# Optimization experiments

Hardware: AMD Instinct MI355X
Metric: run time of the kernel (lower is better)

Reference implementation:

```python
import jax, jax.numpy as jnp
import numpy as np
import math

B, S, H, DM = 1, 2048, 16, 1024
DK = DM // H
MAX_SEQ = 2048  # rel_embed has MAX_SEQ+1 rows


def setup_inputs() -> dict:
    rng = jax.random.key(0)
    ks = jax.random.split(rng, 12)
    w = lambda k, shape, s=0.02: (jax.random.normal(k, shape, jnp.float32) * s)
    inp = {
        'query': jax.random.normal(ks[0], (B, S, DM), jnp.float32),
        'key':   jax.random.normal(ks[1], (B, S, DM), jnp.float32),
        'value': jax.random.normal(ks[2], (B, S, DM), jnp.float32),
        # causal integer mask [B,S,S] (cumsum over it derives rel-pos indices)
        'mask': jnp.broadcast_to(jnp.tril(jnp.ones((S, S), jnp.int32)), (B, S, S)),
        'Wq': w(ks[3], (DM, DM)), 'bq': jnp.zeros((DM,), jnp.float32),
        'Wk': w(ks[4], (DM, DM)), 'bk': jnp.zeros((DM,), jnp.float32),
        'Wv': w(ks[5], (DM, DM)), 'bv': jnp.zeros((DM,), jnp.float32),
        'Wo': w(ks[6], (DM, DM)), 'bo': jnp.zeros((DM,), jnp.float32),
        # relative position embeddings [h, max_seq_len+1, d_k], N(0,1) as in the module
        'rel_embed': jax.random.normal(ks[7], (H, MAX_SEQ + 1, DK), jnp.float32),
    }
    return inp


def reference(query, key, value, mask, Wq, bq, Wk, bk, Wv, bv, Wo, bo, rel_embed):
    scale = 1.0 / math.sqrt(DK)
    heads = lambda x, W, b: (x @ W.T + b).reshape(B, S, H, DK).transpose(0, 2, 1, 3)
    q = heads(query, Wq, bq)   # [B,H,S,DK]
    k = heads(key, Wk, bk)
    v = heads(value, Wv, bv)

    scores = jnp.einsum('bhid,bhjd->bhij', q, k) * scale  # [B,H,S,S]

    m4 = mask[:, None, :, :]                 # [B,1,S,S]
    nz = m4 != 0
    # torch: cumsum(mask)-1 picks the m-index; index 0 (then zeroed) where mask==0
    m_idx = jnp.where(nz, jnp.cumsum(m4, axis=-1) - 1, 0)  # [B,1,S,S]

    # rel_scores[b,h,m,l] = <q[b,h,l,:], rel_embed[h,m,:]> / sqrt(d_k)
    rel = jnp.einsum('bhld,hmd->bhml', q, rel_embed[:, :S]) * scale  # [B,H,S,S]
    idx = jnp.broadcast_to(m_idx, (B, H, S, S))
    # torch.take flat-index decodes to rel[b,h, m_idx[i,j], j]
    rel_g = jnp.take_along_axis(rel, idx, axis=2) * nz.astype(scores.dtype)

    scores = jnp.where(nz, scores + rel_g, jnp.float32(-1e9))
    p = jax.nn.softmax(scores, axis=-1)      # dropout p=0.0 -> identity

    out = jnp.einsum('bhij,bhjd->bhid', p, v)         # [B,H,S,DK]
    out = out.transpose(0, 2, 1, 3).reshape(B, S, DM)  # [B,S,DM]
    return out @ Wo.T + bo
```

## Files before the change

### kernel.cpp

```cpp
#include <hip/hip_runtime.h>

typedef __bf16 bf16_t;
typedef __bf16 bf16x4 __attribute__((ext_vector_type(4)));
typedef __bf16 bf16x8 __attribute__((ext_vector_type(8)));
typedef float  f32x4  __attribute__((ext_vector_type(4)));
typedef float  f32x16 __attribute__((ext_vector_type(16)));
typedef unsigned int u32;

#define S_LEN 2048
#define DMODEL 1024
#define NHEAD 16
#define DHEAD 64
#define RELROWS 2049

__device__ __forceinline__ void gload16(const void* g, void* l) {
    __builtin_amdgcn_global_load_lds((const __attribute__((address_space(1))) void*)g,
                                     (__attribute__((address_space(3))) void*)l,
                                     16, 0, 0);
}

__device__ __forceinline__ f32x4 mfma16(bf16x8 a, bf16x8 b, f32x4 c) {
    return __builtin_amdgcn_mfma_f32_16x16x32_bf16(a, b, c, 0, 0, 0);
}
__device__ __forceinline__ f32x16 mfma32(bf16x8 a, bf16x8 b, f32x16 c) {
    return __builtin_amdgcn_mfma_f32_32x32x16_bf16(a, b, c, 0, 0, 0);
}

__device__ __forceinline__ bf16x8 lds_read_swz(const bf16_t* base, int row, int colb) {
    return *(const bf16x8*)((const char*)base + row * 128 + (colb ^ ((row & 7) << 4)));
}

__device__ __forceinline__ u32 cvtpk(float lo, float hi) {
    u32 w;
    asm("v_cvt_pk_bf16_f32 %0, %1, %2" : "=v"(w) : "v"(lo), "v"(hi));
    return w;
}
__device__ __forceinline__ void swap32(u32& a, u32& b) {
    asm("v_permlane32_swap_b32 %0, %1" : "+v"(a), "+v"(b));
}
__device__ __forceinline__ float fexp2(float x) {
    float r;
    asm("v_exp_f32 %0, %1" : "=v"(r) : "v"(x));
    return r;
}

__global__ __launch_bounds__(256)
void f2bf_all(const float* __restrict__ xq, const float* __restrict__ xk,
              const float* __restrict__ xv,
              const float* __restrict__ wq, const float* __restrict__ wk,
              const float* __restrict__ wv, const float* __restrict__ wo,
              bf16_t* __restrict__ dst, int n4X, int n4W) {
    const int i = blockIdx.x * blockDim.x + threadIdx.x;
    const float* src; int j;
    if (i < 3 * n4X) {
        if (i < n4X)            { src = xq; j = i; }
        else if (i < 2 * n4X)   { src = xk; j = i - n4X; }
        else                    { src = xv; j = i - 2 * n4X; }
    } else {
        int w = i - 3 * n4X;
        if (w < n4W)            { src = wq; j = w; }
        else if (w < 2 * n4W)   { src = wk; j = w - n4W; }
        else if (w < 3 * n4W)   { src = wv; j = w - 2 * n4W; }
        else                    { src = wo; j = w - 3 * n4W; }
    }
    float4 v = ((const float4*)src)[j];
    bf16x4 o;
    o[0] = (bf16_t)v.x; o[1] = (bf16_t)v.y; o[2] = (bf16_t)v.z; o[3] = (bf16_t)v.w;
    ((bf16x4*)dst)[i] = o;
}

template <int BM, int BN>
__global__ __launch_bounds__(256)
void gemm_qkv(const bf16_t* __restrict__ Abase, const bf16_t* __restrict__ Wbase,
              const float* __restrict__ b0, const float* __restrict__ b1,
              const float* __restrict__ b2,
              bf16_t* __restrict__ outb,
              const float* __restrict__ relp, float* __restrict__ RGout,
              bf16_t* __restrict__ vtp,
              int M, int N, int K) {
    __shared__ alignas(16) bf16_t As[2][BM * 64];
    __shared__ alignas(16) bf16_t Bs[2][BN * 64];
    const int tid = threadIdx.x, lane = tid & 63, wave = tid >> 6;
    const int z = blockIdx.z;
    const bf16_t* A = Abase + (size_t)z * M * K;
    const bf16_t* W = Wbase + (size_t)z * N * K;
    const float* bias = (z == 0) ? b0 : (z == 1 ? b1 : b2);
    const int nwg = gridDim.x * gridDim.y;
    const int wg = blockIdx.y * gridDim.x + blockIdx.x;
    const int swz = (wg & 7) * (nwg >> 3) + (wg >> 3);
    const int m0 = (swz / gridDim.x) * BM, n0 = (swz % gridDim.x) * BN;
    const int wr = (wave >> 1) * (BM / 2), wc = (wave & 1) * (BN / 2);
    constexpr int MR = BM / 32, NR = BN / 32;
    constexpr int LOADS = BM / 32 + BN / 32;

    f32x4 acc[MR][NR] = {};
    const int soff = wave * 1024 + lane * 16;

    auto stage = [&](int b, int kt) {
#pragma unroll
        for (int r = 0; r < BM / 32; ++r) {
            int L = r * 4096 + soff;
            int row = L >> 7, colb = (L & 127) ^ ((row & 7) << 4);
            gload16(A + (size_t)(m0 + row) * K + kt + (colb >> 1),
                    (char*)As[b] + r * 4096 + wave * 1024);
        }
#pragma unroll
        for (int r = 0; r < BN / 32; ++r) {
            int L = r * 4096 + soff;
            int row = L >> 7, colb = (L & 127) ^ ((row & 7) << 4);
            gload16(W + (size_t)(n0 + row) * K + kt + (colb >> 1),
                    (char*)Bs[b] + r * 4096 + wave * 1024);
        }
    };

    const int NK = K >> 6;
    stage(0, 0);
    for (int s = 0; s < NK; ++s) {
        const int buf = s & 1;
        if (s + 1 < NK) {
            stage(buf ^ 1, (s + 1) << 6);
            if constexpr (LOADS == 6) asm volatile("s_waitcnt vmcnt(6)" ::: "memory");
            else if constexpr (LOADS == 4) asm volatile("s_waitcnt vmcnt(4)" ::: "memory");
            else asm volatile("s_waitcnt vmcnt(8)" ::: "memory");
        } else {
            asm volatile("s_waitcnt vmcnt(0)" ::: "memory");
        }
        asm volatile("s_barrier" ::: "memory");
#pragma unroll
        for (int kk = 0; kk < 2; ++kk) {
            bf16x8 af[MR], bfr[NR];
#pragma unroll
            for (int m = 0; m < MR; ++m)
                af[m] = lds_read_swz(As[buf], wr + m * 16 + (lane & 15),
                                     kk * 64 + (lane >> 4) * 16);
#pragma unroll
            for (int n = 0; n < NR; ++n)
                bfr[n] = lds_read_swz(Bs[buf], wc + n * 16 + (lane & 15),
                                      kk * 64 + (lane >> 4) * 16);
#pragma unroll
            for (int m = 0; m < MR; ++m)
#pragma unroll
                for (int n = 0; n < NR; ++n)
                    acc[m][n] = mfma16(af[m], bfr[n], acc[m][n]);
        }
        asm volatile("s_barrier" ::: "memory");
    }

    const float scale = (z == 0) ? 0.18033688011112042f : 1.0f;
    float rp[MR][4];
#pragma unroll
    for (int m = 0; m < MR; ++m)
#pragma unroll
        for (int r2 = 0; r2 < 4; ++r2) rp[m][r2] = 0.f;
    const int hh = n0 >> 6;
#pragma unroll
    for (int m = 0; m < MR; ++m) {
        const int gi = m0 + wr + m * 16 + (lane >> 4) * 4;
#pragma unroll
        for (int n = 0; n < NR; ++n) {
            const int gj = n0 + wc + n * 16 + (lane & 15);
            const float bv = bias[gj];
            if (z == 2) {
                bf16x4 o4;
#pragma unroll
                for (int r2 = 0; r2 < 4; ++r2) o4[r2] = (bf16_t)(acc[m][n][r2] + bv);
                *(bf16x4*)&vtp[(size_t)gj * S_LEN + gi] = o4;
            } else {
#pragma unroll
                for (int r2 = 0; r2 < 4; ++r2) {
                    float v = (acc[m][n][r2] + bv) * scale;
                    outb[(size_t)z * M * N + (size_t)(gi + r2) * N + gj] = (bf16_t)v;
                    if (z == 0)
                        rp[m][r2] += v * relp[((size_t)hh * RELROWS + (gi + r2)) * DHEAD + (gj & 63)];
                }
            }
        }
    }
    if (z == 0) {
        constexpr int HM = BM / 2;
        float* Rp = (float*)As;
#pragma unroll
        for (int m = 0; m < MR; ++m)
#pragma unroll
            for (int r2 = 0; r2 < 4; ++r2) {
                float p = rp[m][r2];
                p += __shfl_xor(p, 1);
                p += __shfl_xor(p, 2);
                p += __shfl_xor(p, 4);
                p += __shfl_xor(p, 8);
                if ((lane & 15) == 0)
                    Rp[wave * HM + m * 16 + (lane >> 4) * 4 + r2] = p;
            }
        __syncthreads();
        if ((wave & 1) == 0) {
#pragma unroll
            for (int rr0 = 0; rr0 < HM; rr0 += 64) {
                int rr = rr0 + lane;
                if (rr < HM) {
                    float v = Rp[wave * HM + rr] + Rp[(wave + 1) * HM + rr];
                    RGout[hh * S_LEN + m0 + wr + rr] = v;
                }
            }
        }
    }
}

__global__ __launch_bounds__(512)
void gemm_out(const bf16_t* __restrict__ A, const bf16_t* __restrict__ W,
              const float* __restrict__ bias, float* __restrict__ outf,
              int M, int N, int K) {
    __shared__ alignas(16) bf16_t As[2][2][64 * 64];
    __shared__ alignas(16) bf16_t Bs[2][2][64 * 64];
    const int tid = threadIdx.x, lane = tid & 63, wave = tid >> 6;
    const int grp = wave >> 2, w4 = wave & 3;
    const int nwg = gridDim.x * gridDim.y;
    const int wg = blockIdx.y * gridDim.x + blockIdx.x;
    const int swz = (wg & 7) * (nwg >> 3) + (wg >> 3);
    const int m0 = (swz / gridDim.x) * 64, n0 = (swz % gridDim.x) * 64;
    const int wr = (w4 >> 1) * 32, wc = (w4 & 1) * 32;
    const int kbase = grp * (K >> 1);

    f32x4 acc[2][2] = {};
    const int soff = w4 * 1024 + lane * 16;

    auto stage = [&](int b, int kt) {
#pragma unroll
        for (int r = 0; r < 2; ++r) {
            int L = r * 4096 + soff;
            int row = L >> 7, colb = (L & 127) ^ ((row & 7) << 4);
            gload16(A + (size_t)(m0 + row) * K + kt + (colb >> 1),
                    (char*)As[grp][b] + r * 4096 + w4 * 1024);
            gload16(W + (size_t)(n0 + row) * K + kt + (colb >> 1),
                    (char*)Bs[grp][b] + r * 4096 + w4 * 1024);
        }
    };

    const int NKg = K >> 7;
    stage(0, kbase);
    for (int s = 0; s < NKg; ++s) {
        const int buf = s & 1;
        if (s + 1 < NKg) {
            stage(buf ^ 1, kbase + ((s + 1) << 6));
            asm volatile("s_waitcnt vmcnt(4)" ::: "memory");
        } else {
            asm volatile("s_waitcnt vmcnt(0)" ::: "memory");
        }
        asm volatile("s_barrier" ::: "memory");
#pragma unroll
        for (int kk = 0; kk < 2; ++kk) {
            bf16x8 af[2], bfr[2];
#pragma unroll
            for (int m = 0; m < 2; ++m)
                af[m] = lds_read_swz(As[grp][buf], wr + m * 16 + (lane & 15),
                                     kk * 64 + (lane >> 4) * 16);
#pragma unroll
            for (int n = 0; n < 2; ++n)
                bfr[n] = lds_read_swz(Bs[grp][buf], wc + n * 16 + (lane & 15),
                                      kk * 64 + (lane >> 4) * 16);
#pragma unroll
            for (int m = 0; m < 2; ++m)
#pragma unroll
                for (int n = 0; n < 2; ++n)
                    acc[m][n] = mfma16(af[m], bfr[n], acc[m][n]);
        }
        asm volatile("s_barrier" ::: "memory");
    }

    float* scr = (float*)As;
    if (grp == 1) {
        float* base = scr + ((w4 * 64 + lane) << 4);
#pragma unroll
        for (int m = 0; m < 2; ++m)
#pragma unroll
            for (int n = 0; n < 2; ++n)
                *(f32x4*)(base + (m * 2 + n) * 4) = acc[m][n];
    }
    __syncthreads();
    if (grp == 0) {
        const float* base = scr + ((w4 * 64 + lane) << 4);
#pragma unroll
        for (int m = 0; m < 2; ++m) {
            const int gi = m0 + wr + m * 16 + (lane >> 4) * 4;
#pragma unroll
            for (int n = 0; n < 2; ++n) {
                f32x4 ov = *(const f32x4*)(base + (m * 2 + n) * 4);
                const int gj = n0 + wc + n * 16 + (lane & 15);
                const float bv = bias[gj];
#pragma unroll
                for (int r2 = 0; r2 < 4; ++r2)
                    outf[(size_t)(gi + r2) * N + gj] = acc[m][n][r2] + ov[r2] + bv;
            }
        }
    }
}

__global__ __launch_bounds__(256, 2)
void flash_attn(const bf16_t* __restrict__ Qb, const bf16_t* __restrict__ Kb,
                const bf16_t* __restrict__ Vtp, const float* __restrict__ RG,
                bf16_t* __restrict__ Ob) {
    __shared__ alignas(16) bf16_t KB[4][64 * 64];
    __shared__ alignas(16) bf16_t VB[4][64 * 64];
    __shared__ alignas(16) float Rs[S_LEN];
    const int tid = threadIdx.x, lane = tid & 63, wave = tid >> 6;
    const int h = blockIdx.x;
    const int qt = (int)gridDim.y - 1 - (int)blockIdx.y;
    const int q0 = qt * 32;
    const int nt = (qt >> 1) + 1;
    const int qpar = qt & 1;
    const int lo5 = lane & 31, hi = lane >> 5;

    const int nkv = nt * 64;
    for (int i = tid * 8; i < nkv; i += 2048) {
        *(float4*)&Rs[i]     = *(const float4*)&RG[h * S_LEN + i];
        *(float4*)&Rs[i + 4] = *(const float4*)&RG[h * S_LEN + i + 4];
    }

    const bf16_t* qp = Qb + (size_t)(q0 + lo5) * DMODEL + h * DHEAD;
    bf16x8 qf[4];
#pragma unroll
    for (int c = 0; c < 4; ++c)
        qf[c] = *(const bf16x8*)(qp + c * 16 + hi * 8);

    auto stageK = [&](int tt) {
        char* dst = (char*)KB[wave];
#pragma unroll
        for (int rr = 0; rr < 8; ++rr) {
            int L = rr * 1024 + lane * 16;
            int row = L >> 7, colb = (L & 127) ^ ((row & 7) << 4);
            gload16(Kb + (size_t)(tt * 64 + row) * DMODEL + h * DHEAD + (colb >> 1),
                    dst + rr * 1024);
        }
    };
    auto stageV = [&](int tt) {
        char* dst = (char*)VB[wave];
#pragma unroll
        for (int rr = 0; rr < 8; ++rr) {
            int L = rr * 1024 + lane * 16;
            int row = L >> 7, colb = (L & 127) ^ ((row & 7) << 4);
            gload16(Vtp + (size_t)(h * DHEAD + row) * S_LEN + tt * 64 + (colb >> 1),
                    dst + rr * 1024);
        }
    };

    if (wave < nt) { stageK(wave); stageV(wave); }
    __syncthreads();

    f32x16 oacc[2] = {};
    float ls = 0.f;
    const int thr = qpar * 32 + lo5;

    for (int tt = wave; tt < nt; tt += 4) {
        const int kv0 = tt * 64;
        const bool diag = (tt == nt - 1);
        asm volatile("s_waitcnt vmcnt(8)" ::: "memory");

        f32x16 sta, stb;
#pragma unroll
        for (int g = 0; g < 4; ++g) {
            f32x4 ra = *(const f32x4*)&Rs[kv0 + g * 8 + hi * 4];
            f32x4 rb = *(const f32x4*)&Rs[kv0 + 32 + g * 8 + hi * 4];
#pragma unroll
            for (int e = 0; e < 4; ++e) { sta[g * 4 + e] = ra[e]; stb[g * 4 + e] = rb[e]; }
        }
        __builtin_amdgcn_s_setprio(1);
#pragma unroll
        for (int c = 0; c < 4; ++c) {
            bf16x8 kfa = lds_read_swz(KB[wave], lo5, c * 32 + hi * 16);
            sta = mfma32(kfa, qf[c], sta);
        }
#pragma unroll
        for (int c = 0; c < 4; ++c) {
            bf16x8 kfb = lds_read_swz(KB[wave], 32 + lo5, c * 32 + hi * 16);
            stb = mfma32(kfb, qf[c], stb);
        }
        __builtin_amdgcn_s_setprio(0);
        if (tt + 4 < nt) stageK(tt + 4);

        float pra[16], prb[16];
        if (diag) {
#pragma unroll
            for (int r = 0; r < 16; ++r) {
                int kloc = (r & 3) + 8 * (r >> 2) + 4 * hi;
                float va = fexp2(sta[r]), vb = fexp2(stb[r]);
                pra[r] = (kloc > thr) ? 0.f : va;
                prb[r] = (kloc + 32 > thr) ? 0.f : vb;
            }
        } else {
#pragma unroll
            for (int r = 0; r < 16; ++r) { pra[r] = fexp2(sta[r]); prb[r] = fexp2(stb[r]); }
        }
#pragma unroll
        for (int r = 0; r < 16; ++r) ls += pra[r] + prb[r];
        u32 pw[4][4];
#pragma unroll
        for (int hf = 0; hf < 2; ++hf) {
            u32 a  = cvtpk(pra[8 * hf + 0], pra[8 * hf + 1]);
            u32 b  = cvtpk(pra[8 * hf + 4], pra[8 * hf + 5]);
            swap32(a, b);
            u32 c2 = cvtpk(pra[8 * hf + 2], pra[8 * hf + 3]);
            u32 d2 = cvtpk(pra[8 * hf + 6], pra[8 * hf + 7]);
            swap32(c2, d2);
            pw[hf][0] = a;  pw[hf][1] = c2;  pw[hf][2] = b;  pw[hf][3] = d2;
        }
#pragma unroll
        for (int hf = 0; hf < 2; ++hf) {
            u32 a  = cvtpk(prb[8 * hf + 0], prb[8 * hf + 1]);
            u32 b  = cvtpk(prb[8 * hf + 4], prb[8 * hf + 5]);
            swap32(a, b);
            u32 c2 = cvtpk(prb[8 * hf + 2], prb[8 * hf + 3]);
            u32 d2 = cvtpk(prb[8 * hf + 6], prb[8 * hf + 7]);
            swap32(c2, d2);
            pw[2 + hf][0] = a;  pw[2 + hf][1] = c2;  pw[2 + hf][2] = b;  pw[2 + hf][3] = d2;
        }

        if (tt + 4 < nt) asm volatile("s_waitcnt vmcnt(8)" ::: "memory");
        else             asm volatile("s_waitcnt vmcnt(0)" ::: "memory");

        __builtin_amdgcn_s_setprio(1);
#pragma unroll
        for (int kc = 0; kc < 4; ++kc) {
            union { u32 w[4]; bf16x8 v; } uu;
            uu.w[0] = pw[kc][0]; uu.w[1] = pw[kc][1]; uu.w[2] = pw[kc][2]; uu.w[3] = pw[kc][3];
#pragma unroll
            for (int db = 0; db < 2; ++db) {
                bf16x8 vf = lds_read_swz(VB[wave], db * 32 + lo5, kc * 32 + hi * 16);
                oacc[db] = mfma32(vf, uu.v, oacc[db]);
            }
        }
        __builtin_amdgcn_s_setprio(0);
        if (tt + 4 < nt) stageV(tt + 4);
    }

    asm volatile("s_waitcnt vmcnt(0)" ::: "memory");
    __syncthreads();
    float* scr = (float*)KB;
    if (wave > 0) {
        float* base = scr + (wave - 1) * 2112 + lane * 32;
#pragma unroll
        for (int db = 0; db < 2; ++db)
#pragma unroll
            for (int g = 0; g < 4; ++g) {
                f32x4 v4;
#pragma unroll
                for (int e = 0; e < 4; ++e) v4[e] = oacc[db][g * 4 + e];
                *(f32x4*)(base + db * 16 + g * 4) = v4;
            }
        scr[(wave - 1) * 2112 + 2048 + lane] = ls;
    }
    __syncthreads();
    if (wave == 0) {
#pragma unroll
        for (int w2 = 0; w2 < 3; ++w2) {
            const float* base = scr + w2 * 2112 + lane * 32;
#pragma unroll
            for (int db = 0; db < 2; ++db)
#pragma unroll
                for (int g = 0; g < 4; ++g) {
                    f32x4 v4 = *(const f32x4*)(base + db * 16 + g * 4);
#pragma unroll
                    for (int e = 0; e < 4; ++e) oacc[db][g * 4 + e] += v4[e];
                }
            ls += scr[w2 * 2112 + 2048 + lane];
        }
        ls += __shfl_xor(ls, 32);
        const float inv = 1.0f / ls;
        const int qg = q0 + lo5;
#pragma unroll
        for (int db = 0; db < 2; ++db)
#pragma unroll
            for (int g = 0; g < 4; ++g) {
                bf16x4 o4;
#pragma unroll
                for (int e = 0; e < 4; ++e)
                    o4[e] = (bf16_t)(oacc[db][g * 4 + e] * inv);
                *(bf16x4*)&Ob[(size_t)qg * DMODEL + h * DHEAD + db * 32 + g * 8 + hi * 4] = o4;
            }
    }
}

extern "C" void kernel_launch(void* const* d_in, const int* in_sizes, int n_in,
                              void* d_out, int out_size, void* d_ws, size_t ws_size,
                              hipStream_t stream) {
    const float* query = (const float*)d_in[0];
    const float* key   = (const float*)d_in[1];
    const float* value = (const float*)d_in[2];
    const float* Wq  = (const float*)d_in[4];
    const float* bq  = (const float*)d_in[5];
    const float* Wk  = (const float*)d_in[6];
    const float* bk  = (const float*)d_in[7];
    const float* Wv  = (const float*)d_in[8];
    const float* bv  = (const float*)d_in[9];
    const float* Wo  = (const float*)d_in[10];
    const float* bo  = (const float*)d_in[11];
    const float* rel = (const float*)d_in[12];

    char* ws = (char*)d_ws;
    const size_t nX = (size_t)S_LEN * DMODEL;
    const size_t nW = (size_t)DMODEL * DMODEL;
    bf16_t* Xbf  = (bf16_t*)ws;
    bf16_t* Wbf  = (bf16_t*)(ws + 3 * nX * 2);
    bf16_t* QKV  = (bf16_t*)(ws + 3 * nX * 2 + 4 * nW * 2);
    float*  RG   = (float*)(ws + 3 * nX * 2 + 4 * nW * 2 + 3 * nX * 2);
    bf16_t* Vtp  = QKV + 2 * nX;
    bf16_t* AOb  = (bf16_t*)(ws + nX * 2);
    (void)in_sizes; (void)n_in; (void)out_size; (void)ws_size;

    const int n4X = (int)(nX / 4), n4W = (int)(nW / 4);
    const int tot4 = 3 * n4X + 4 * n4W;
    f2bf_all<<<tot4 / 256, 256, 0, stream>>>(query, key, value, Wq, Wk, Wv, Wo,
                                             Xbf, n4X, n4W);

    gemm_qkv<64, 64><<<dim3(DMODEL / 64, S_LEN / 64, 3), 256, 0, stream>>>(
        Xbf, Wbf, bq, bk, bv, QKV, rel, RG, Vtp, S_LEN, DMODEL, DMODEL);

    flash_attn<<<dim3(NHEAD, S_LEN / 32), 256, 0, stream>>>(QKV, QKV + nX, Vtp, RG, AOb);

    gemm_out<<<dim3(DMODEL / 64, S_LEN / 64), 512, 0, stream>>>(
        AOb, Wbf + 3 * nW, bo, (float*)d_out, S_LEN, DMODEL, DMODEL);
}
```

Measured before the change: 79.11 us.

## Fuse fp32-to-bf16 activation conversion into QKV GEMM A-tile loading

The separate conversion pass over the query/key/value activations is removed. The QKV GEMM now loads fp32 A tiles into registers, converts them with packed bf16 conversion, and writes them swizzled into LDS, while weights still use async global-to-LDS loads. This saves a full write and re-read of 3 bf16 activation tensors plus part of one kernel launch. In exchange, A-tile traffic doubles inside the GEMM and the software pipeline is restructured with register staging, which adds register pressure and extra barriers.

```diff
diff --git a/kernel.cpp b/kernel.cpp
--- a/kernel.cpp
+++ b/kernel.cpp
@@ -6,6 +6,7 @@
 typedef float  f32x4  __attribute__((ext_vector_type(4)));
 typedef float  f32x16 __attribute__((ext_vector_type(16)));
 typedef unsigned int u32;
+typedef u32 u32x4 __attribute__((ext_vector_type(4)));
 
 #define S_LEN 2048
 #define DMODEL 1024
@@ -45,24 +46,15 @@
 }
 
 __global__ __launch_bounds__(256)
-void f2bf_all(const float* __restrict__ xq, const float* __restrict__ xk,
-              const float* __restrict__ xv,
-              const float* __restrict__ wq, const float* __restrict__ wk,
-              const float* __restrict__ wv, const float* __restrict__ wo,
-              bf16_t* __restrict__ dst, int n4X, int n4W) {
+void f2bf_w(const float* __restrict__ wq, const float* __restrict__ wk,
+            const float* __restrict__ wv, const float* __restrict__ wo,
+            bf16_t* __restrict__ dst, int n4W) {
     const int i = blockIdx.x * blockDim.x + threadIdx.x;
     const float* src; int j;
-    if (i < 3 * n4X) {
-        if (i < n4X)            { src = xq; j = i; }
-        else if (i < 2 * n4X)   { src = xk; j = i - n4X; }
-        else                    { src = xv; j = i - 2 * n4X; }
-    } else {
-        int w = i - 3 * n4X;
-        if (w < n4W)            { src = wq; j = w; }
-        else if (w < 2 * n4W)   { src = wk; j = w - n4W; }
-        else if (w < 3 * n4W)   { src = wv; j = w - 2 * n4W; }
-        else                    { src = wo; j = w - 3 * n4W; }
-    }
+    if (i < n4W)            { src = wq; j = i; }
+    else if (i < 2 * n4W)   { src = wk; j = i - n4W; }
+    else if (i < 3 * n4W)   { src = wv; j = i - 2 * n4W; }
+    else                    { src = wo; j = i - 3 * n4W; }
     float4 v = ((const float4*)src)[j];
     bf16x4 o;
     o[0] = (bf16_t)v.x; o[1] = (bf16_t)v.y; o[2] = (bf16_t)v.z; o[3] = (bf16_t)v.w;
@@ -71,7 +63,8 @@
 
 template <int BM, int BN>
 __global__ __launch_bounds__(256)
-void gemm_qkv(const bf16_t* __restrict__ Abase, const bf16_t* __restrict__ Wbase,
+void gemm_qkv(const float* __restrict__ Aq, const float* __restrict__ Ak,
+              const float* __restrict__ Av, const bf16_t* __restrict__ Wbase,
               const float* __restrict__ b0, const float* __restrict__ b1,
               const float* __restrict__ b2,
               bf16_t* __restrict__ outb,
@@ -82,7 +75,7 @@
     __shared__ alignas(16) bf16_t Bs[2][BN * 64];
     const int tid = threadIdx.x, lane = tid & 63, wave = tid >> 6;
     const int z = blockIdx.z;
-    const bf16_t* A = Abase + (size_t)z * M * K;
+    const float* A = (z == 0) ? Aq : (z == 1 ? Ak : Av);
     const bf16_t* W = Wbase + (size_t)z * N * K;
     const float* bias = (z == 0) ? b0 : (z == 1 ? b1 : b2);
     const int nwg = gridDim.x * gridDim.y;
@@ -91,19 +84,31 @@
     const int m0 = (swz / gridDim.x) * BM, n0 = (swz % gridDim.x) * BN;
     const int wr = (wave >> 1) * (BM / 2), wc = (wave & 1) * (BN / 2);
     constexpr int MR = BM / 32, NR = BN / 32;
-    constexpr int LOADS = BM / 32 + BN / 32;
 
     f32x4 acc[MR][NR] = {};
     const int soff = wave * 1024 + lane * 16;
 
-    auto stage = [&](int b, int kt) {
-#pragma unroll
-        for (int r = 0; r < BM / 32; ++r) {
-            int L = r * 4096 + soff;
-            int row = L >> 7, colb = (L & 127) ^ ((row & 7) << 4);
-            gload16(A + (size_t)(m0 + row) * K + kt + (colb >> 1),
-                    (char*)As[b] + r * 4096 + wave * 1024);
-        }
+    const int arow = tid >> 2, acol = (tid & 3) * 16;
+    float4 av0, av1, av2, av3;
+    auto loadA = [&](int kt) {
+        const float* src = A + (size_t)(m0 + arow) * K + kt + acol;
+        av0 = *(const float4*)(src + 0);
+        av1 = *(const float4*)(src + 4);
+        av2 = *(const float4*)(src + 8);
+        av3 = *(const float4*)(src + 12);
+    };
+    auto writeA = [&](int b) {
+        u32x4 w0, w1;
+        w0[0] = cvtpk(av0.x, av0.y); w0[1] = cvtpk(av0.z, av0.w);
+        w0[2] = cvtpk(av1.x, av1.y); w0[3] = cvtpk(av1.z, av1.w);
+        w1[0] = cvtpk(av2.x, av2.y); w1[1] = cvtpk(av2.z, av2.w);
+        w1[2] = cvtpk(av3.x, av3.y); w1[3] = cvtpk(av3.z, av3.w);
+        char* base = (char*)As[b] + arow * 128;
+        const int sw = (arow & 7) << 4;
+        *(u32x4*)(base + (((tid & 3) * 32) ^ sw))      = w0;
+        *(u32x4*)(base + (((tid & 3) * 32 + 16) ^ sw)) = w1;
+    };
+    auto stageW = [&](int b, int kt) {
 #pragma unroll
         for (int r = 0; r < BN / 32; ++r) {
             int L = r * 4096 + soff;
@@ -114,18 +119,14 @@
     };
 
     const int NK = K >> 6;
-    stage(0, 0);
+    loadA(0); stageW(0, 0);
+    writeA(0);
+    loadA(64); stageW(1, 64);
+    asm volatile("s_waitcnt vmcnt(6)" ::: "memory");
+    asm volatile("s_waitcnt lgkmcnt(0)\n\ts_barrier" ::: "memory");
+
     for (int s = 0; s < NK; ++s) {
         const int buf = s & 1;
-        if (s + 1 < NK) {
-            stage(buf ^ 1, (s + 1) << 6);
-            if constexpr (LOADS == 6) asm volatile("s_waitcnt vmcnt(6)" ::: "memory");
-            else if constexpr (LOADS == 4) asm volatile("s_waitcnt vmcnt(4)" ::: "memory");
-            else asm volatile("s_waitcnt vmcnt(8)" ::: "memory");
-        } else {
-            asm volatile("s_waitcnt vmcnt(0)" ::: "memory");
-        }
-        asm volatile("s_barrier" ::: "memory");
 #pragma unroll
         for (int kk = 0; kk < 2; ++kk) {
             bf16x8 af[MR], bfr[NR];
@@ -143,7 +144,18 @@
                 for (int n = 0; n < NR; ++n)
                     acc[m][n] = mfma16(af[m], bfr[n], acc[m][n]);
         }
-        asm volatile("s_barrier" ::: "memory");
+        if (s + 1 < NK) {
+            asm volatile("s_barrier" ::: "memory");
+            writeA(buf ^ 1);
+            if (s + 2 < NK) {
+                loadA((s + 2) << 6);
+                stageW(buf, (s + 2) << 6);
+                asm volatile("s_waitcnt vmcnt(6)" ::: "memory");
+            } else {
+                asm volatile("s_waitcnt vmcnt(0)" ::: "memory");
+            }
+            asm volatile("s_waitcnt lgkmcnt(0)\n\ts_barrier" ::: "memory");
+        }
     }
 
     const float scale = (z == 0) ? 0.18033688011112042f : 1.0f;
@@ -178,6 +190,7 @@
     }
     if (z == 0) {
         constexpr int HM = BM / 2;
+        __syncthreads();
         float* Rp = (float*)As;
 #pragma unroll
         for (int m = 0; m < MR; ++m)
@@ -497,7 +510,6 @@
     char* ws = (char*)d_ws;
     const size_t nX = (size_t)S_LEN * DMODEL;
     const size_t nW = (size_t)DMODEL * DMODEL;
-    bf16_t* Xbf  = (bf16_t*)ws;
     bf16_t* Wbf  = (bf16_t*)(ws + 3 * nX * 2);
     bf16_t* QKV  = (bf16_t*)(ws + 3 * nX * 2 + 4 * nW * 2);
     float*  RG   = (float*)(ws + 3 * nX * 2 + 4 * nW * 2 + 3 * nX * 2);
@@ -505,13 +517,11 @@
     bf16_t* AOb  = (bf16_t*)(ws + nX * 2);
     (void)in_sizes; (void)n_in; (void)out_size; (void)ws_size;
 
-    const int n4X = (int)(nX / 4), n4W = (int)(nW / 4);
-    const int tot4 = 3 * n4X + 4 * n4W;
-    f2bf_all<<<tot4 / 256, 256, 0, stream>>>(query, key, value, Wq, Wk, Wv, Wo,
-                                             Xbf, n4X, n4W);
+    const int n4W = (int)(nW / 4);
+    f2bf_w<<<(4 * n4W) / 256, 256, 0, stream>>>(Wq, Wk, Wv, Wo, Wbf, n4W);
 
     gemm_qkv<64, 64><<<dim3(DMODEL / 64, S_LEN / 64, 3), 256, 0, stream>>>(
-        Xbf, Wbf, bq, bk, bv, QKV, rel, RG, Vtp, S_LEN, DMODEL, DMODEL);
+        query, key, value, Wbf, bq, bk, bv, QKV, rel, RG, Vtp, S_LEN, DMODEL, DMODEL);
 
     flash_attn<<<dim3(NHEAD, S_LEN / 32), 256, 0, stream>>>(QKV, QKV + nX, Vtp, RG, AOb);
 
```

After: 91.30 us. 15.4% more time.
